# Kernel optimization log

Measured on AMD Instinct MI355X. Metric: run time of the kernel, lower is better.

Reference implementation:

```python
import jax, jax.numpy as jnp
import numpy as np

B = 16384
IN = 512
A = 16
E = 9  # 9 position-specific experts
H1, H2, H3 = 512, 256, 128


def setup_inputs() -> dict:
    key = jax.random.key(0)
    ks = jax.random.split(key, 10)
    s = lambda fan_in: 1.0 / np.sqrt(fan_in)
    return {
        "x": jax.random.normal(ks[0], (B, IN), dtype=jnp.float32),
        "position": jax.random.randint(ks[1], (B,), 0, 9, dtype=jnp.int64),
        # torch Linear convention: W [out, in], y = x @ W.T + b; stacked per expert [E, out, in]
        "W1": jax.random.uniform(ks[2], (E, H1, IN), jnp.float32, -s(IN), s(IN)),
        "b1": jax.random.uniform(ks[3], (E, H1), jnp.float32, -s(IN), s(IN)),
        "W2": jax.random.uniform(ks[4], (E, H2, H1), jnp.float32, -s(H1), s(H1)),
        "b2": jax.random.uniform(ks[5], (E, H2), jnp.float32, -s(H1), s(H1)),
        "W3": jax.random.uniform(ks[6], (E, H3, H2), jnp.float32, -s(H2), s(H2)),
        "b3": jax.random.uniform(ks[7], (E, H3), jnp.float32, -s(H2), s(H2)),
        "W4": jax.random.uniform(ks[8], (E, A, H3), jnp.float32, -s(H3), s(H3)),
        "b4": jax.random.uniform(ks[9], (E, A), jnp.float32, -s(H3), s(H3)),
    }


def reference(x, position, W1, b1, W2, b2, W3, b3, W4, b4):
    # Each sample i is routed through expert min(position[i], 8).
    # Dense MoE reference: run all 9 experts over the full batch, then
    # select the routed expert's logits per sample (same math as the
    # per-sample Python loop in the original module).
    pos = jnp.minimum(position, 8)
    h = jax.nn.relu(jnp.einsum('bi,eoi->ebo', x, W1) + b1[:, None, :])   # [E,B,H1]
    h = jax.nn.relu(jnp.einsum('ebi,eoi->ebo', h, W2) + b2[:, None, :])  # [E,B,H2]
    h = jax.nn.relu(jnp.einsum('ebi,eoi->ebo', h, W3) + b3[:, None, :])  # [E,B,H3]
    logits_all = jnp.einsum('ebi,eoi->ebo', h, W4) + b4[:, None, :]      # [E,B,A]
    logits = logits_all[pos, jnp.arange(x.shape[0])]                     # [B,A]
    return jax.nn.softmax(logits, axis=1)
```

## Files before the change

kernel.cpp:

```cpp
#include <hip/hip_runtime.h>

typedef _Float16 f16;
typedef __attribute__((ext_vector_type(8))) _Float16 f16x8;
typedef __attribute__((ext_vector_type(4))) _Float16 f16x4;
typedef __attribute__((ext_vector_type(4))) float f32x4;

#define MFMA16(a, b, c) __builtin_amdgcn_mfma_f32_16x16x32_f16(a, b, c, 0, 0, 0)

#define B_N 16384
#define E_N 9
#define TILE 32
#define NTILE_MAX 520
#define THREADS 512

#define D_IN 512
#define D_H1 512
#define D_H2 256
#define D_H3 128
#define D_A 16

#define RPW 104
#define O4B 7667712
#define WPL_BYTES 7704576
#define WSLOTS (WPL_BYTES / 16)

#define IDX_OFF 64
#define WP_OFF 131584

#define H2_OFF 32768
#define RING_OFF 49152
#define LDS_BYTES 73728


__global__ void k_bucket(const int* __restrict__ pos, int* __restrict__ hdr,
                         int* __restrict__ idx) {
  __shared__ int cnt[E_N], cur[E_N];
  __shared__ int flag_s;
  const int t = threadIdx.x;
  if (t < E_N) cnt[t] = 0;
  if (t == 0) {
    int nz = 0;
    for (int i = 0; i < 64; ++i) nz |= pos[2 * i + 1];
    flag_s = (nz == 0) ? 1 : 0;
  }
  __syncthreads();
  const bool f64 = flag_s != 0;
  int e[16];
#pragma unroll
  for (int k = 0; k < 16; ++k) {
    int i = k * 1024 + t;
    long long v = f64 ? ((const long long*)pos)[i] : (long long)pos[i];
    v = v < 0 ? 0 : (v > 8 ? 8 : v);
    e[k] = (int)v;
    atomicAdd(&cnt[e[k]], 1);
  }
  __syncthreads();
  if (t == 0) {
    int acc = 0;
    for (int ee = 0; ee < E_N; ++ee) { cur[ee] = acc; acc += cnt[ee]; }
  }
  if (t < E_N) hdr[8 + t] = cnt[t];
  __syncthreads();
#pragma unroll
  for (int k = 0; k < 16; ++k) {
    int i = k * 1024 + t;
    int slot = atomicAdd(&cur[e[k]], 1);
    idx[slot] = i;
  }
}


__global__ void k_wcvt(const float* __restrict__ W1, const float* __restrict__ W2,
                       const float* __restrict__ W3, const float* __restrict__ W4,
                       char* __restrict__ wp) {
  int slot = blockIdx.x * 256 + threadIdx.x;
  if (slot >= WSLOTS) return;
  long addr = (long)slot << 4;
  int lane = slot & 63;
  int lg = lane >> 4, ln = lane & 15;
  const float* src;
  if (addr < O4B) {
    int rec = (int)(addr >> 10);
    int f = rec % RPW;
    int ew = rec / RPW;
    int w = ew & 7, e = ew >> 3;
    if (f < 64) {
      int kk = f >> 2, nf = f & 3;
      int n = w * 64 + nf * 16 + ln;
      int k = kk * 32 + lg * 8;
      src = W1 + ((long)e * D_H1 + n) * D_IN + k;
    } else if (f < 96) {
      int j = f - 64;
      int kk = j >> 1, nf = j & 1;
      int n = w * 32 + nf * 16 + ln;
      int k = kk * 32 + lg * 8;
      src = W2 + ((long)e * D_H2 + n) * D_H1 + k;
    } else {
      int kk = f - 96;
      int n = w * 16 + ln;
      int k = kk * 32 + lg * 8;
      src = W3 + ((long)e * D_H3 + n) * D_H2 + k;
    }
  } else {
    long rel = addr - O4B;
    int e = (int)(rel >> 12);
    int r2 = (int)(rel & 4095);
    int s = r2 >> 4, n = s >> 4, k16 = s & 15;
    src = W4 + ((long)e * D_A + n) * D_H3 + k16 * 8;
  }
  float4 a = *(const float4*)src;
  float4 b = *(const float4*)(src + 4);
  f16x8 h;
  h[0] = (f16)a.x; h[1] = (f16)a.y; h[2] = (f16)a.z; h[3] = (f16)a.w;
  h[4] = (f16)b.x; h[5] = (f16)b.y; h[6] = (f16)b.z; h[7] = (f16)b.w;
  *(f16x8*)(wp + addr) = h;
}


__device__ __forceinline__ f16x8 afrag(const char* base, int strideB, int rowoff,
                                       int kbytes, int lane) {
  int m = rowoff + (lane & 15);
  int q = kbytes + ((lane >> 4) * 16);
  return *(const f16x8*)(base + m * strideB + (q ^ ((m & 15) << 4)));
}

__device__ __forceinline__ void dma16(const char* g, char* l) {
  __builtin_amdgcn_global_load_lds(
      (const __attribute__((address_space(1))) void*)g,
      (__attribute__((address_space(3))) void*)l, 16, 0, 0);
}

template <int N> __device__ __forceinline__ void waitv();
template <> __device__ __forceinline__ void waitv<2>() {
  asm volatile("s_waitcnt vmcnt(2)" ::: "memory");
}
template <> __device__ __forceinline__ void waitv<1>() {
  asm volatile("s_waitcnt vmcnt(1)" ::: "memory");
}
template <> __device__ __forceinline__ void waitv<0>() {
  asm volatile("s_waitcnt vmcnt(0)" ::: "memory");
}

__launch_bounds__(THREADS, 2)
__global__ void k_mlp(const float* __restrict__ x,
                      const float* __restrict__ b1, const float* __restrict__ b2,
                      const float* __restrict__ b3, const float* __restrict__ b4,
                      const int* __restrict__ hdr, const int* __restrict__ idx,
                      const char* __restrict__ wp, float* __restrict__ out) {
  __shared__ __align__(16) char lds[LDS_BYTES];

  int b = blockIdx.x;
  int bswz = (b & 7) * (NTILE_MAX / 8) + (b >> 3);

  const int* counts = hdr + 8;
  int e = -1, tile = 0, base = 0, ne = 0;
  {
    int acc = 0, off = 0;
    for (int ee = 0; ee < E_N; ++ee) {
      int n = counts[ee];
      int nt = (n + TILE - 1) / TILE;
      if (bswz < acc + nt) { e = ee; tile = bswz - acc; ne = n; base = off; break; }
      acc += nt; off += n;
    }
  }
  if (e < 0) return;
  const int rvalid = min(TILE, ne - tile * TILE);
  const int row0 = base + tile * TILE;

  const int t = threadIdx.x;
  const int lane = t & 63;
  const int wid = t >> 6;
  const int lg = lane >> 4;
  const int ln = lane & 15;

  const char* wb = wp + ((long)(e * 8 + wid) * RPW << 10);
  const char* wpe4 = wp + O4B + (long)e * 4096;
  char* ringw = lds + RING_OFF + wid * 3072;

  dma16(wb + 0 * 1024 + lane * 16, ringw + 0 * 1024);
  dma16(wb + 1 * 1024 + lane * 16, ringw + 1 * 1024);
  dma16(wb + 2 * 1024 + lane * 16, ringw + 2 * 1024);

  const float4* x4 = (const float4*)x;
#pragma unroll
  for (int v8 = 0; v8 < 8; ++v8) {
    int u = v8 * THREADS + t;
    int s = u >> 7, c4 = u & 127;
    float4 v = make_float4(0.f, 0.f, 0.f, 0.f);
    if (s < rvalid) v = x4[(long)idx[row0 + s] * (D_IN / 4) + c4];
    f16x4 h;
    h[0] = (f16)v.x; h[1] = (f16)v.y; h[2] = (f16)v.z; h[3] = (f16)v.w;
    *(f16x4*)(lds + s * 1024 + ((c4 * 8) ^ ((s & 15) << 4))) = h;
  }
  __syncthreads();

  {
    f32x4 acc[2][4];
#pragma unroll
    for (int m = 0; m < 2; ++m)
#pragma unroll
      for (int nf = 0; nf < 4; ++nf) acc[m][nf] = (f32x4){0.f, 0.f, 0.f, 0.f};

#pragma unroll
    for (int kk = 0; kk < 16; ++kk) {
      f16x8 A0 = afrag(lds, 1024, 0, kk * 64, lane);
      f16x8 A1 = afrag(lds, 1024, 16, kk * 64, lane);
#pragma unroll
      for (int nf = 0; nf < 4; ++nf) {
        const int rec = kk * 4 + nf;
        waitv<2>();
        f16x8 B = *(const f16x8*)(ringw + (rec % 3) * 1024 + lane * 16);
        __builtin_amdgcn_s_setprio(1);
        acc[0][nf] = MFMA16(A0, B, acc[0][nf]);
        acc[1][nf] = MFMA16(A1, B, acc[1][nf]);
        __builtin_amdgcn_s_setprio(0);
        const int nr = rec + 3;
        dma16(wb + (long)nr * 1024 + lane * 16, ringw + (nr % 3) * 1024);
      }
    }
    __syncthreads();

#pragma unroll
    for (int nf = 0; nf < 4; ++nf) {
      int n = wid * 64 + nf * 16 + ln;
      float bias = b1[e * D_H1 + n];
#pragma unroll
      for (int m = 0; m < 2; ++m)
#pragma unroll
        for (int j = 0; j < 4; ++j) {
          float v = acc[m][nf][j] + bias;
          v = v > 0.f ? v : 0.f;
          int rw = m * 16 + lg * 4 + j;
          *(f16*)(lds + rw * 1024 + ((n * 2) ^ ((rw & 15) << 4))) = (f16)v;
        }
    }
  }
  __syncthreads();

  {
    f32x4 acc2[2][2];
#pragma unroll
    for (int m = 0; m < 2; ++m)
#pragma unroll
      for (int nf = 0; nf < 2; ++nf) acc2[m][nf] = (f32x4){0.f, 0.f, 0.f, 0.f};

#pragma unroll
    for (int kk = 0; kk < 16; ++kk) {
      f16x8 A0 = afrag(lds, 1024, 0, kk * 64, lane);
      f16x8 A1 = afrag(lds, 1024, 16, kk * 64, lane);
#pragma unroll
      for (int nf = 0; nf < 2; ++nf) {
        const int rec = 64 + kk * 2 + nf;
        waitv<2>();
        f16x8 B = *(const f16x8*)(ringw + (rec % 3) * 1024 + lane * 16);
        __builtin_amdgcn_s_setprio(1);
        acc2[0][nf] = MFMA16(A0, B, acc2[0][nf]);
        acc2[1][nf] = MFMA16(A1, B, acc2[1][nf]);
        __builtin_amdgcn_s_setprio(0);
        const int nr = rec + 3;
        dma16(wb + (long)nr * 1024 + lane * 16, ringw + (nr % 3) * 1024);
      }
    }
#pragma unroll
    for (int nf = 0; nf < 2; ++nf) {
      int n = wid * 32 + nf * 16 + ln;
      float bias = b2[e * D_H2 + n];
#pragma unroll
      for (int m = 0; m < 2; ++m)
#pragma unroll
        for (int j = 0; j < 4; ++j) {
          float v = acc2[m][nf][j] + bias;
          v = v > 0.f ? v : 0.f;
          int rw = m * 16 + lg * 4 + j;
          *(f16*)(lds + H2_OFF + rw * 512 + ((n * 2) ^ ((rw & 15) << 4))) = (f16)v;
        }
    }
  }
  __syncthreads();

  {
    f32x4 acc3[2];
    acc3[0] = (f32x4){0.f, 0.f, 0.f, 0.f};
    acc3[1] = (f32x4){0.f, 0.f, 0.f, 0.f};

#define L3STEP(REC, WAITN)                                                     \
  {                                                                            \
    const int kk3 = (REC) - 96;                                                \
    f16x8 A0 = afrag(lds + H2_OFF, 512, 0, kk3 * 64, lane);                    \
    f16x8 A1 = afrag(lds + H2_OFF, 512, 16, kk3 * 64, lane);                   \
    waitv<WAITN>();                                                            \
    f16x8 B = *(const f16x8*)(ringw + ((REC) % 3) * 1024 + lane * 16);         \
    __builtin_amdgcn_s_setprio(1);                                             \
    acc3[0] = MFMA16(A0, B, acc3[0]);                                          \
    acc3[1] = MFMA16(A1, B, acc3[1]);                                          \
    __builtin_amdgcn_s_setprio(0);                                             \
    if ((REC) + 3 <= 103)                                                      \
      dma16(wb + (long)((REC) + 3) * 1024 + lane * 16,                         \
            ringw + (((REC) + 3) % 3) * 1024);                                 \
  }

    L3STEP(96, 2)
    L3STEP(97, 2)
    L3STEP(98, 2)
    L3STEP(99, 2)
    L3STEP(100, 2)
    L3STEP(101, 2)
    L3STEP(102, 1)
    L3STEP(103, 0)
#undef L3STEP

    int n = wid * 16 + ln;
    float bias = b3[e * D_H3 + n];
#pragma unroll
    for (int m = 0; m < 2; ++m)
#pragma unroll
      for (int j = 0; j < 4; ++j) {
        float v = acc3[m][j] + bias;
        v = v > 0.f ? v : 0.f;
        int rw = m * 16 + lg * 4 + j;
        *(f16*)(lds + rw * 256 + ((n * 2) ^ ((rw & 15) << 4))) = (f16)v;
      }
  }
  __syncthreads();

  if (wid < 2) {
    f32x4 a4 = (f32x4){0.f, 0.f, 0.f, 0.f};
#pragma unroll
    for (int kc = 0; kc < 4; ++kc) {
      f16x8 Bv = *(const f16x8*)(wpe4 + ln * 256 + kc * 64 + lg * 16);
      f16x8 Av = afrag(lds, 256, wid * 16, kc * 64, lane);
      a4 = MFMA16(Av, Bv, a4);
    }
    float bias = b4[e * D_A + ln];
#pragma unroll
    for (int j = 0; j < 4; ++j) {
      float v = a4[j] + bias;
      float mx = v;
      for (int msk = 8; msk >= 1; msk >>= 1) mx = fmaxf(mx, __shfl_xor(mx, msk));
      float pe = expf(v - mx);
      float sm = pe;
      for (int msk = 8; msk >= 1; msk >>= 1) sm += __shfl_xor(sm, msk);
      int rl = wid * 16 + lg * 4 + j;
      if (rl < rvalid) out[(long)idx[row0 + rl] * D_A + ln] = pe / sm;
    }
  }
}


extern "C" void kernel_launch(void* const* d_in, const int* in_sizes, int n_in,
                              void* d_out, int out_size, void* d_ws, size_t ws_size,
                              hipStream_t stream) {
  const float* x  = (const float*)d_in[0];
  const int* pos  = (const int*)d_in[1];
  const float* W1 = (const float*)d_in[2];
  const float* b1 = (const float*)d_in[3];
  const float* W2 = (const float*)d_in[4];
  const float* b2 = (const float*)d_in[5];
  const float* W3 = (const float*)d_in[6];
  const float* b3 = (const float*)d_in[7];
  const float* W4 = (const float*)d_in[8];
  const float* b4 = (const float*)d_in[9];
  float* out = (float*)d_out;

  int* hdr = (int*)d_ws;
  int* idx = hdr + IDX_OFF;
  char* wp = (char*)d_ws + WP_OFF;

  hipLaunchKernelGGL(k_bucket, dim3(1), dim3(1024), 0, stream, pos, hdr, idx);
  hipLaunchKernelGGL(k_wcvt, dim3(WSLOTS / 256), dim3(256), 0, stream,
                     W1, W2, W3, W4, wp);
  hipLaunchKernelGGL(k_mlp, dim3(NTILE_MAX), dim3(THREADS), 0, stream,
                     x, b1, b2, b3, b4, hdr, idx, wp, out);
}
```

Measured before the change: 67.94 us.

## Use 16 waves per block with register-prefetched weight fragments instead of LDS DMA ring

Doubles the block to 1024 threads so each of 16 waves owns half as many output columns per layer, and repacks the weight layout into per-wave record streams (56 records for the first 8 waves, 48 for the rest, which skip layer 3). The LDS ring fed by global_load_lds DMA with explicit vmcnt waits is replaced by a 4-deep register queue of direct global loads, which frees 24KB of LDS. The aim is more latency hiding and less LDS traffic and waiting per wave. The cost is higher register pressure at 1024 threads with launch bounds of 2 blocks, idle waves during layer 3, and reliance on the compiler to schedule the waits for the register loads.

```diff
diff --git a/kernel.cpp b/kernel.cpp
--- a/kernel.cpp
+++ b/kernel.cpp
@@ -11,7 +11,7 @@
 #define E_N 9
 #define TILE 32
 #define NTILE_MAX 520
-#define THREADS 512
+#define THREADS 1024
 
 #define D_IN 512
 #define D_H1 512
@@ -19,7 +19,6 @@
 #define D_H3 128
 #define D_A 16
 
-#define RPW 104
 #define O4B 7667712
 #define WPL_BYTES 7704576
 #define WSLOTS (WPL_BYTES / 16)
@@ -28,8 +27,7 @@
 #define WP_OFF 131584
 
 #define H2_OFF 32768
-#define RING_OFF 49152
-#define LDS_BYTES 73728
+#define LDS_BYTES 49152
 
 
 __global__ void k_bucket(const int* __restrict__ pos, int* __restrict__ hdr,
@@ -76,29 +74,27 @@
   int slot = blockIdx.x * 256 + threadIdx.x;
   if (slot >= WSLOTS) return;
   long addr = (long)slot << 4;
-  int lane = slot & 63;
+  int lane = (int)((addr >> 4) & 63);
   int lg = lane >> 4, ln = lane & 15;
   const float* src;
   if (addr < O4B) {
     int rec = (int)(addr >> 10);
-    int f = rec % RPW;
-    int ew = rec / RPW;
-    int w = ew & 7, e = ew >> 3;
-    if (f < 64) {
-      int kk = f >> 2, nf = f & 3;
-      int n = w * 64 + nf * 16 + ln;
-      int k = kk * 32 + lg * 8;
+    int e = rec / 832;
+    int q = rec - e * 832;
+    int s, r;
+    if (q < 448) { s = q / 56; r = q - s * 56; }
+    else { int q2 = q - 448; s = 8 + q2 / 48; r = q2 - (s - 8) * 48; }
+    if (r < 32) {
+      int n = s * 32 + (r & 1) * 16 + ln;
+      int k = (r >> 1) * 32 + lg * 8;
       src = W1 + ((long)e * D_H1 + n) * D_IN + k;
-    } else if (f < 96) {
-      int j = f - 64;
-      int kk = j >> 1, nf = j & 1;
-      int n = w * 32 + nf * 16 + ln;
-      int k = kk * 32 + lg * 8;
+    } else if (r < 48) {
+      int n = s * 16 + ln;
+      int k = (r - 32) * 32 + lg * 8;
       src = W2 + ((long)e * D_H2 + n) * D_H1 + k;
     } else {
-      int kk = f - 96;
-      int n = w * 16 + ln;
-      int k = kk * 32 + lg * 8;
+      int n = (s & 7) * 16 + ln;
+      int k = (r - 48) * 32 + lg * 8;
       src = W3 + ((long)e * D_H3 + n) * D_H2 + k;
     }
   } else {
@@ -124,21 +120,8 @@
   return *(const f16x8*)(base + m * strideB + (q ^ ((m & 15) << 4)));
 }
 
-__device__ __forceinline__ void dma16(const char* g, char* l) {
-  __builtin_amdgcn_global_load_lds(
-      (const __attribute__((address_space(1))) void*)g,
-      (__attribute__((address_space(3))) void*)l, 16, 0, 0);
-}
-
-template <int N> __device__ __forceinline__ void waitv();
-template <> __device__ __forceinline__ void waitv<2>() {
-  asm volatile("s_waitcnt vmcnt(2)" ::: "memory");
-}
-template <> __device__ __forceinline__ void waitv<1>() {
-  asm volatile("s_waitcnt vmcnt(1)" ::: "memory");
-}
-template <> __device__ __forceinline__ void waitv<0>() {
-  asm volatile("s_waitcnt vmcnt(0)" ::: "memory");
+__device__ __forceinline__ f16x8 ldfrag(const char* wb, int f, int lane) {
+  return *(const f16x8*)(wb + (long)f * 1024 + lane * 16);
 }
 
 __launch_bounds__(THREADS, 2)
@@ -173,17 +156,19 @@
   const int lg = lane >> 4;
   const int ln = lane & 15;
 
-  const char* wb = wp + ((long)(e * 8 + wid) * RPW << 10);
+  const char* wb = wp + ((long)e * 832 +
+                         (wid < 8 ? wid * 56 : 448 + (wid - 8) * 48)) * 1024;
   const char* wpe4 = wp + O4B + (long)e * 4096;
-  char* ringw = lds + RING_OFF + wid * 3072;
-
-  dma16(wb + 0 * 1024 + lane * 16, ringw + 0 * 1024);
-  dma16(wb + 1 * 1024 + lane * 16, ringw + 1 * 1024);
-  dma16(wb + 2 * 1024 + lane * 16, ringw + 2 * 1024);
+
+  f16x8 Q[4];
+  Q[0] = ldfrag(wb, 0, lane);
+  Q[1] = ldfrag(wb, 1, lane);
+  Q[2] = ldfrag(wb, 2, lane);
+  Q[3] = ldfrag(wb, 3, lane);
 
   const float4* x4 = (const float4*)x;
 #pragma unroll
-  for (int v8 = 0; v8 < 8; ++v8) {
+  for (int v8 = 0; v8 < 4; ++v8) {
     int u = v8 * THREADS + t;
     int s = u >> 7, c4 = u & 127;
     float4 v = make_float4(0.f, 0.f, 0.f, 0.f);
@@ -194,121 +179,91 @@
   }
   __syncthreads();
 
+  f32x4 acc[2][2];
+#pragma unroll
+  for (int m = 0; m < 2; ++m)
+#pragma unroll
+    for (int nf = 0; nf < 2; ++nf) acc[m][nf] = (f32x4){0.f, 0.f, 0.f, 0.f};
+
+#pragma unroll
+  for (int kk = 0; kk < 16; ++kk) {
+    f16x8 A0 = afrag(lds, 1024, 0, kk * 64, lane);
+    f16x8 A1 = afrag(lds, 1024, 16, kk * 64, lane);
+#pragma unroll
+    for (int nf = 0; nf < 2; ++nf) {
+      const int r = kk * 2 + nf;
+      f16x8 B = Q[r & 3];
+      __builtin_amdgcn_s_setprio(1);
+      acc[0][nf] = MFMA16(A0, B, acc[0][nf]);
+      acc[1][nf] = MFMA16(A1, B, acc[1][nf]);
+      __builtin_amdgcn_s_setprio(0);
+      Q[r & 3] = ldfrag(wb, r + 4, lane);
+    }
+  }
+  __syncthreads();
+
+#pragma unroll
+  for (int nf = 0; nf < 2; ++nf) {
+    int n = wid * 32 + nf * 16 + ln;
+    float bias = b1[e * D_H1 + n];
+#pragma unroll
+    for (int m = 0; m < 2; ++m)
+#pragma unroll
+      for (int j = 0; j < 4; ++j) {
+        float v = acc[m][nf][j] + bias;
+        v = v > 0.f ? v : 0.f;
+        int rw = m * 16 + lg * 4 + j;
+        *(f16*)(lds + rw * 1024 + ((n * 2) ^ ((rw & 15) << 4))) = (f16)v;
+      }
+  }
+  __syncthreads();
+
   {
-    f32x4 acc[2][4];
-#pragma unroll
-    for (int m = 0; m < 2; ++m)
-#pragma unroll
-      for (int nf = 0; nf < 4; ++nf) acc[m][nf] = (f32x4){0.f, 0.f, 0.f, 0.f};
-
+    f32x4 acc2[2];
+    acc2[0] = (f32x4){0.f, 0.f, 0.f, 0.f};
+    acc2[1] = (f32x4){0.f, 0.f, 0.f, 0.f};
 #pragma unroll
     for (int kk = 0; kk < 16; ++kk) {
       f16x8 A0 = afrag(lds, 1024, 0, kk * 64, lane);
       f16x8 A1 = afrag(lds, 1024, 16, kk * 64, lane);
-#pragma unroll
-      for (int nf = 0; nf < 4; ++nf) {
-        const int rec = kk * 4 + nf;
-        waitv<2>();
-        f16x8 B = *(const f16x8*)(ringw + (rec % 3) * 1024 + lane * 16);
-        __builtin_amdgcn_s_setprio(1);
-        acc[0][nf] = MFMA16(A0, B, acc[0][nf]);
-        acc[1][nf] = MFMA16(A1, B, acc[1][nf]);
-        __builtin_amdgcn_s_setprio(0);
-        const int nr = rec + 3;
-        dma16(wb + (long)nr * 1024 + lane * 16, ringw + (nr % 3) * 1024);
+      const int r = 32 + kk;
+      f16x8 B = Q[r & 3];
+      __builtin_amdgcn_s_setprio(1);
+      acc2[0] = MFMA16(A0, B, acc2[0]);
+      acc2[1] = MFMA16(A1, B, acc2[1]);
+      __builtin_amdgcn_s_setprio(0);
+      Q[r & 3] = ldfrag(wb, r + 4, lane);
+    }
+    int n = wid * 16 + ln;
+    float bias = b2[e * D_H2 + n];
+#pragma unroll
+    for (int m = 0; m < 2; ++m)
+#pragma unroll
+      for (int j = 0; j < 4; ++j) {
+        float v = acc2[m][j] + bias;
+        v = v > 0.f ? v : 0.f;
+        int rw = m * 16 + lg * 4 + j;
+        *(f16*)(lds + H2_OFF + rw * 512 + ((n * 2) ^ ((rw & 15) << 4))) = (f16)v;
       }
-    }
-    __syncthreads();
-
-#pragma unroll
-    for (int nf = 0; nf < 4; ++nf) {
-      int n = wid * 64 + nf * 16 + ln;
-      float bias = b1[e * D_H1 + n];
-#pragma unroll
-      for (int m = 0; m < 2; ++m)
-#pragma unroll
-        for (int j = 0; j < 4; ++j) {
-          float v = acc[m][nf][j] + bias;
-          v = v > 0.f ? v : 0.f;
-          int rw = m * 16 + lg * 4 + j;
-          *(f16*)(lds + rw * 1024 + ((n * 2) ^ ((rw & 15) << 4))) = (f16)v;
-        }
-    }
-  }
-  __syncthreads();
-
-  {
-    f32x4 acc2[2][2];
-#pragma unroll
-    for (int m = 0; m < 2; ++m)
-#pragma unroll
-      for (int nf = 0; nf < 2; ++nf) acc2[m][nf] = (f32x4){0.f, 0.f, 0.f, 0.f};
-
-#pragma unroll
-    for (int kk = 0; kk < 16; ++kk) {
-      f16x8 A0 = afrag(lds, 1024, 0, kk * 64, lane);
-      f16x8 A1 = afrag(lds, 1024, 16, kk * 64, lane);
-#pragma unroll
-      for (int nf = 0; nf < 2; ++nf) {
-        const int rec = 64 + kk * 2 + nf;
-        waitv<2>();
-        f16x8 B = *(const f16x8*)(ringw + (rec % 3) * 1024 + lane * 16);
-        __builtin_amdgcn_s_setprio(1);
-        acc2[0][nf] = MFMA16(A0, B, acc2[0][nf]);
-        acc2[1][nf] = MFMA16(A1, B, acc2[1][nf]);
-        __builtin_amdgcn_s_setprio(0);
-        const int nr = rec + 3;
-        dma16(wb + (long)nr * 1024 + lane * 16, ringw + (nr % 3) * 1024);
-      }
-    }
-#pragma unroll
-    for (int nf = 0; nf < 2; ++nf) {
-      int n = wid * 32 + nf * 16 + ln;
-      float bias = b2[e * D_H2 + n];
-#pragma unroll
-      for (int m = 0; m < 2; ++m)
-#pragma unroll
-        for (int j = 0; j < 4; ++j) {
-          float v = acc2[m][nf][j] + bias;
-          v = v > 0.f ? v : 0.f;
-          int rw = m * 16 + lg * 4 + j;
-          *(f16*)(lds + H2_OFF + rw * 512 + ((n * 2) ^ ((rw & 15) << 4))) = (f16)v;
-        }
-    }
-  }
-  __syncthreads();
-
-  {
+  }
+  __syncthreads();
+
+  if (wid < 8) {
     f32x4 acc3[2];
     acc3[0] = (f32x4){0.f, 0.f, 0.f, 0.f};
     acc3[1] = (f32x4){0.f, 0.f, 0.f, 0.f};
-
-#define L3STEP(REC, WAITN)                                                     \
-  {                                                                            \
-    const int kk3 = (REC) - 96;                                                \
-    f16x8 A0 = afrag(lds + H2_OFF, 512, 0, kk3 * 64, lane);                    \
-    f16x8 A1 = afrag(lds + H2_OFF, 512, 16, kk3 * 64, lane);                   \
-    waitv<WAITN>();                                                            \
-    f16x8 B = *(const f16x8*)(ringw + ((REC) % 3) * 1024 + lane * 16);         \
-    __builtin_amdgcn_s_setprio(1);                                             \
-    acc3[0] = MFMA16(A0, B, acc3[0]);                                          \
-    acc3[1] = MFMA16(A1, B, acc3[1]);                                          \
-    __builtin_amdgcn_s_setprio(0);                                             \
-    if ((REC) + 3 <= 103)                                                      \
-      dma16(wb + (long)((REC) + 3) * 1024 + lane * 16,                         \
-            ringw + (((REC) + 3) % 3) * 1024);                                 \
-  }
-
-    L3STEP(96, 2)
-    L3STEP(97, 2)
-    L3STEP(98, 2)
-    L3STEP(99, 2)
-    L3STEP(100, 2)
-    L3STEP(101, 2)
-    L3STEP(102, 1)
-    L3STEP(103, 0)
-#undef L3STEP
-
+#pragma unroll
+    for (int kk = 0; kk < 8; ++kk) {
+      const int r = 48 + kk;
+      f16x8 A0 = afrag(lds + H2_OFF, 512, 0, kk * 64, lane);
+      f16x8 A1 = afrag(lds + H2_OFF, 512, 16, kk * 64, lane);
+      f16x8 B = Q[r & 3];
+      __builtin_amdgcn_s_setprio(1);
+      acc3[0] = MFMA16(A0, B, acc3[0]);
+      acc3[1] = MFMA16(A1, B, acc3[1]);
+      __builtin_amdgcn_s_setprio(0);
+      if (r + 4 <= 55) Q[r & 3] = ldfrag(wb, r + 4, lane);
+    }
     int n = wid * 16 + ln;
     float bias = b3[e * D_H3 + n];
 #pragma unroll
```

After: 70.86 us. 4.3% more time.

## Split fused per-tile MLP into per-layer grouped GEMMs with 128-row tiles

Applied to the files above, without the earlier changes.

Replaces the single fused 32-row-tile MLP kernel with a pipeline: an x gather/convert kernel into a padded, swizzled fp16 buffer, three grouped GEMM kernels (128x128 tiles, double-buffered LDS) that convert weights inline, and a scalar layer-4 softmax kernel. Larger row tiles raise weight reuse per load and remove the separate weight pre-conversion pass. In exchange it adds intermediate activation round-trips through global memory and extra launches. The fused path is kept as a fallback when the workspace is too small.

```diff
diff --git a/kernel.cpp b/kernel.cpp
--- a/kernel.cpp
+++ b/kernel.cpp
@@ -9,9 +9,8 @@
 
 #define B_N 16384
 #define E_N 9
-#define TILE 32
-#define NTILE_MAX 520
-#define THREADS 512
+#define MAXT 144
+#define MP_MAX 17536
 
 #define D_IN 512
 #define D_H1 512
@@ -19,17 +18,41 @@
 #define D_H3 128
 #define D_A 16
 
-#define RPW 104
-#define O4B 7667712
-#define WPL_BYTES 7704576
-#define WSLOTS (WPL_BYTES / 16)
-
-#define IDX_OFF 64
-#define WP_OFF 131584
-
-#define H2_OFF 32768
-#define RING_OFF 49152
-#define LDS_BYTES 73728
+#define IDX_I 64
+#define SIDX_B 65792
+#define XG_B 136192
+#define H1_B 18093056
+#define H2_B 136192
+#define H3_B 9114624
+#define WS_NEED_PIPE 36049920ull
+#define F_RPW 104
+#define F_O4B 7667712
+#define F_WPL 7704576
+#define F_WSLOTS (F_WPL / 16)
+#define F_WP_OFF 131584
+#define F_H2_OFF 32768
+#define F_RING_OFF 49152
+#define F_LDS 73728
+#define F_NTILE 520
+
+
+
+__device__ __forceinline__ void dma16(const char* g, char* l) {
+  __builtin_amdgcn_global_load_lds(
+      (const __attribute__((address_space(1))) void*)g,
+      (__attribute__((address_space(3))) void*)l, 16, 0, 0);
+}
+
+template <int N> __device__ __forceinline__ void waitv();
+template <> __device__ __forceinline__ void waitv<2>() {
+  asm volatile("s_waitcnt vmcnt(2)" ::: "memory");
+}
+template <> __device__ __forceinline__ void waitv<1>() {
+  asm volatile("s_waitcnt vmcnt(1)" ::: "memory");
+}
+template <> __device__ __forceinline__ void waitv<0>() {
+  asm volatile("s_waitcnt vmcnt(0)" ::: "memory");
+}
 
 
 __global__ void k_bucket(const int* __restrict__ pos, int* __restrict__ hdr,
@@ -56,10 +79,22 @@
   }
   __syncthreads();
   if (t == 0) {
-    int acc = 0;
-    for (int ee = 0; ee < E_N; ++ee) { cur[ee] = acc; acc += cnt[ee]; }
-  }
-  if (t < E_N) hdr[8 + t] = cnt[t];
+    int ua = 0, pa = 0, ta = 0;
+    for (int ee = 0; ee < E_N; ++ee) {
+      cur[ee] = ua;
+      hdr[8 + ee] = cnt[ee];
+      hdr[20 + ee] = ua;
+      hdr[32 + ee] = pa;
+      hdr[44 + ee] = ta;
+      int c = cnt[ee];
+      ua += c;
+      int tl = (c + 127) >> 7;
+      pa += tl << 7;
+      ta += tl;
+    }
+    hdr[32 + 9] = pa;
+    hdr[44 + 9] = ta;
+  }
   __syncthreads();
 #pragma unroll
   for (int k = 0; k < 16; ++k) {
@@ -70,19 +105,221 @@
 }
 
 
-__global__ void k_wcvt(const float* __restrict__ W1, const float* __restrict__ W2,
-                       const float* __restrict__ W3, const float* __restrict__ W4,
-                       char* __restrict__ wp) {
+__global__ void k_xcvt(const float* __restrict__ x, const int* __restrict__ hdr,
+                       const int* __restrict__ idx, char* __restrict__ xg,
+                       int* __restrict__ sidx) {
+  const int* cnt = hdr + 8;
+  const int* uoff = hdr + 20;
+  const int* pof = hdr + 32;
+  const int Mp = pof[9];
+  int gtid = blockIdx.x * 256 + threadIdx.x;
+
+  if (gtid < MP_MAX) {
+    int v = -1;
+    if (gtid < Mp) {
+      int e = 0;
+#pragma unroll
+      for (int ee = 1; ee < E_N; ++ee) if (gtid >= pof[ee]) e = ee;
+      int i = gtid - pof[e];
+      if (i < cnt[e]) v = idx[uoff[e] + i];
+    }
+    sidx[gtid] = v;
+  }
+
+  if (gtid >= Mp * 64) return;
+  long L = (long)gtid << 4;
+  int c = (int)(L >> 14);
+  int tile = c >> 3, ks = c & 7;
+  int r = (int)((L >> 7) & 127);
+  int pos = (int)(L & 127);
+  int slot = (tile << 7) + r;
+  int klog = pos ^ ((r & 7) << 4);
+  int k = (ks << 6) + (klog >> 1);
+
+  int e = 0;
+#pragma unroll
+  for (int ee = 1; ee < E_N; ++ee) if (slot >= pof[ee]) e = ee;
+  int i = slot - pof[e];
+  f16x8 h;
+  if (i < cnt[e]) {
+    int orig = idx[uoff[e] + i];
+    const float* src = x + (long)orig * D_IN + k;
+    float4 a = *(const float4*)src;
+    float4 b = *(const float4*)(src + 4);
+    h[0] = (f16)a.x; h[1] = (f16)a.y; h[2] = (f16)a.z; h[3] = (f16)a.w;
+    h[4] = (f16)b.x; h[5] = (f16)b.y; h[6] = (f16)b.z; h[7] = (f16)b.w;
+  } else {
+#pragma unroll
+    for (int q = 0; q < 8; ++q) h[q] = (f16)0.f;
+  }
+  *(f16x8*)(xg + L) = h;
+}
+
+__device__ __forceinline__ f16x8 afragP(const char* base, int rowoff, int kbytes,
+                                        int lane) {
+  int m = rowoff + (lane & 15);
+  int q = kbytes + ((lane >> 4) * 16);
+  return *(const f16x8*)(base + m * 128 + (q ^ ((m & 7) << 4)));
+}
+
+template <int K, int NTN>
+__launch_bounds__(512, 2)
+__global__ void k_gemm(const char* __restrict__ Ag, const float* __restrict__ W,
+                       const float* __restrict__ bias, const int* __restrict__ hdr,
+                       char* __restrict__ Og) {
+  constexpr int NOUT = NTN * 128;
+  constexpr int S = K / 64;
+  constexpr int OCH = NOUT / 64;
+  __shared__ __align__(16) char lds[65536];
+
+  const int* pof = hdr + 32;
+  const int* ptil = hdr + 44;
+  int nb = blockIdx.x;
+  int tb = nb / NTN, nt = nb % NTN;
+  if (tb >= ptil[9]) return;
+  int e = 0;
+#pragma unroll
+  for (int ee = 1; ee < E_N; ++ee) if (tb >= ptil[ee]) e = ee;
+  const int slot0 = pof[e] + (tb - ptil[e]) * 128;
+
+  const int t = threadIdx.x;
+  const int lane = t & 63;
+  const int wid = t >> 6;
+  const int lg = lane >> 4;
+  const int ln = lane & 15;
+  const int mw = wid >> 1;
+  const int nw = wid & 1;
+
+  const char* Abase = Ag + (((long)(slot0 >> 7) * S) << 14);
+
+  auto stageA = [&](int s, int p) {
+    const char* src = Abase + ((long)s << 14) + wid * 1024 + lane * 16;
+    char* d0 = lds + p * 16384 + wid * 1024;
+    dma16(src, d0);
+    dma16(src + 8192, d0 + 8192);
+  };
+  auto stageW = [&](int s, int p) {
+    char* wd = lds + 32768 + p * 16384;
+#pragma unroll
+    for (int j = 0; j < 2; ++j) {
+      int q = t + j * 512;
+      int col = q >> 3, kb16 = q & 7;
+      int klog = (kb16 * 16) ^ ((col & 7) << 4);
+      int k = s * 64 + (klog >> 1);
+      const float* wsrc = W + ((long)(e * NOUT + nt * 128 + col) * K + k);
+      float4 a = *(const float4*)wsrc;
+      float4 b = *(const float4*)(wsrc + 4);
+      f16x8 h;
+      h[0] = (f16)a.x; h[1] = (f16)a.y; h[2] = (f16)a.z; h[3] = (f16)a.w;
+      h[4] = (f16)b.x; h[5] = (f16)b.y; h[6] = (f16)b.z; h[7] = (f16)b.w;
+      *(f16x8*)(wd + q * 16) = h;
+    }
+  };
+
+  f32x4 acc[2][4];
+#pragma unroll
+  for (int m2 = 0; m2 < 2; ++m2)
+#pragma unroll
+    for (int nf = 0; nf < 4; ++nf) acc[m2][nf] = (f32x4){0.f, 0.f, 0.f, 0.f};
+
+  stageA(0, 0);
+  stageW(0, 0);
+  __syncthreads();
+
+  for (int s = 0; s < S; ++s) {
+    const int p = s & 1;
+    if (s + 1 < S) { stageA(s + 1, p ^ 1); stageW(s + 1, p ^ 1); }
+    const char* Ap = lds + p * 16384;
+    const char* Wp = lds + 32768 + p * 16384;
+#pragma unroll
+    for (int ks = 0; ks < 2; ++ks) {
+      f16x8 A0 = afragP(Ap, mw * 32, ks * 64, lane);
+      f16x8 A1 = afragP(Ap, mw * 32 + 16, ks * 64, lane);
+#pragma unroll
+      for (int nf = 0; nf < 4; ++nf) {
+        f16x8 B = afragP(Wp, nw * 64 + nf * 16, ks * 64, lane);
+        acc[0][nf] = MFMA16(A0, B, acc[0][nf]);
+        acc[1][nf] = MFMA16(A1, B, acc[1][nf]);
+      }
+    }
+    __syncthreads();
+  }
+
+#pragma unroll
+  for (int nf = 0; nf < 4; ++nf) {
+    int cg = nt * 128 + nw * 64 + nf * 16 + ln;
+    float bb = bias[e * NOUT + cg];
+#pragma unroll
+    for (int m2 = 0; m2 < 2; ++m2)
+#pragma unroll
+      for (int j = 0; j < 4; ++j) {
+        float v = acc[m2][nf][j] + bb;
+        v = v > 0.f ? v : 0.f;
+        int row = mw * 32 + m2 * 16 + lg * 4 + j;
+        int slot = slot0 + row;
+        long byte = ((long)((slot >> 7) * OCH + (cg >> 6)) << 14) +
+                    (long)(slot & 127) * 128 +
+                    (((cg & 63) * 2) ^ ((slot & 7) << 4));
+        *(f16*)(Og + byte) = (f16)v;
+      }
+  }
+}
+
+__global__ void k_l4(const char* __restrict__ h3, const float* __restrict__ W4,
+                     const float* __restrict__ b4, const int* __restrict__ hdr,
+                     const int* __restrict__ sidx, float* __restrict__ out) {
+  const int* pof = hdr + 32;
+  const int* ptil = hdr + 44;
+  int tb = blockIdx.x;
+  if (tb >= ptil[9]) return;
+  int e = 0;
+#pragma unroll
+  for (int ee = 1; ee < E_N; ++ee) if (tb >= ptil[ee]) e = ee;
+  const int slot0 = pof[e] + (tb - ptil[e]) * 128;
+
+  const int t = threadIdx.x;
+  const int rr = t >> 4, a = t & 15;
+#pragma unroll
+  for (int g = 0; g < 8; ++g) {
+    int slot = slot0 + g * 16 + rr;
+    float accv = b4[e * D_A + a];
+#pragma unroll
+    for (int c = 0; c < 16; ++c) {
+      long byte = ((long)((slot >> 7) * 2 + (c >> 3)) << 14) +
+                  (long)(slot & 127) * 128 +
+                  (((c & 7) * 16) ^ ((slot & 7) << 4));
+      f16x8 h = *(const f16x8*)(h3 + byte);
+      const float* w = W4 + ((long)(e * D_A + a) * D_H3 + c * 8);
+      float4 wa = *(const float4*)w;
+      float4 wb = *(const float4*)(w + 4);
+      accv += (float)h[0] * wa.x + (float)h[1] * wa.y + (float)h[2] * wa.z +
+              (float)h[3] * wa.w + (float)h[4] * wb.x + (float)h[5] * wb.y +
+              (float)h[6] * wb.z + (float)h[7] * wb.w;
+    }
+    float mx = accv;
+    for (int msk = 8; msk >= 1; msk >>= 1) mx = fmaxf(mx, __shfl_xor(mx, msk, 16));
+    float pe = expf(accv - mx);
+    float sm = pe;
+    for (int msk = 8; msk >= 1; msk >>= 1) sm += __shfl_xor(sm, msk, 16);
+    int orig = sidx[slot];
+    if (orig >= 0) out[(long)orig * D_A + a] = pe / sm;
+  }
+}
+
+
+__global__ void k_wcvt_f(const float* __restrict__ W1, const float* __restrict__ W2,
+                         const float* __restrict__ W3, const float* __restrict__ W4,
+                         char* __restrict__ wp) {
   int slot = blockIdx.x * 256 + threadIdx.x;
-  if (slot >= WSLOTS) return;
+  if (slot >= F_WSLOTS) return;
   long addr = (long)slot << 4;
   int lane = slot & 63;
   int lg = lane >> 4, ln = lane & 15;
   const float* src;
-  if (addr < O4B) {
+  if (addr < F_O4B) {
     int rec = (int)(addr >> 10);
-    int f = rec % RPW;
-    int ew = rec / RPW;
+    int f = rec % F_RPW;
+    int ew = rec / F_RPW;
     int w = ew & 7, e = ew >> 3;
     if (f < 64) {
       int kk = f >> 2, nf = f & 3;
@@ -102,7 +339,7 @@
       src = W3 + ((long)e * D_H3 + n) * D_H2 + k;
     }
   } else {
-    long rel = addr - O4B;
+    long rel = addr - F_O4B;
     int e = (int)(rel >> 12);
     int r2 = (int)(rel & 4095);
     int s = r2 >> 4, n = s >> 4, k16 = s & 15;
@@ -116,41 +353,23 @@
   *(f16x8*)(wp + addr) = h;
 }
 
-
-__device__ __forceinline__ f16x8 afrag(const char* base, int strideB, int rowoff,
-                                       int kbytes, int lane) {
+__device__ __forceinline__ f16x8 afragS(const char* base, int strideB, int rowoff,
+                                        int kbytes, int lane) {
   int m = rowoff + (lane & 15);
   int q = kbytes + ((lane >> 4) * 16);
   return *(const f16x8*)(base + m * strideB + (q ^ ((m & 15) << 4)));
 }
 
-__device__ __forceinline__ void dma16(const char* g, char* l) {
-  __builtin_amdgcn_global_load_lds(
-      (const __attribute__((address_space(1))) void*)g,
-      (__attribute__((address_space(3))) void*)l, 16, 0, 0);
-}
-
-template <int N> __device__ __forceinline__ void waitv();
-template <> __device__ __forceinline__ void waitv<2>() {
-  asm volatile("s_waitcnt vmcnt(2)" ::: "memory");
-}
-template <> __device__ __forceinline__ void waitv<1>() {
-  asm volatile("s_waitcnt vmcnt(1)" ::: "memory");
-}
-template <> __device__ __forceinline__ void waitv<0>() {
-  asm volatile("s_waitcnt vmcnt(0)" ::: "memory");
-}
-
-__launch_bounds__(THREADS, 2)
-__global__ void k_mlp(const float* __restrict__ x,
-                      const float* __restrict__ b1, const float* __restrict__ b2,
-                      const float* __restrict__ b3, const float* __restrict__ b4,
-                      const int* __restrict__ hdr, const int* __restrict__ idx,
-                      const char* __restrict__ wp, float* __restrict__ out) {
-  __shared__ __align__(16) char lds[LDS_BYTES];
+__launch_bounds__(512, 2)
+__global__ void k_mlp_f(const float* __restrict__ x,
+                        const float* __restrict__ b1, const float* __restrict__ b2,
+                        const float* __restrict__ b3, const float* __restrict__ b4,
+                        const int* __restrict__ hdr, const int* __restrict__ idx,
+                        const char* __restrict__ wp, float* __restrict__ out) {
+  __shared__ __align__(16) char lds[F_LDS];
 
   int b = blockIdx.x;
-  int bswz = (b & 7) * (NTILE_MAX / 8) + (b >> 3);
+  int bswz = (b & 7) * (F_NTILE / 8) + (b >> 3);
 
   const int* counts = hdr + 8;
   int e = -1, tile = 0, base = 0, ne = 0;
@@ -158,14 +377,14 @@
     int acc = 0, off = 0;
     for (int ee = 0; ee < E_N; ++ee) {
       int n = counts[ee];
-      int nt = (n + TILE - 1) / TILE;
+      int nt = (n + 31) / 32;
       if (bswz < acc + nt) { e = ee; tile = bswz - acc; ne = n; base = off; break; }
       acc += nt; off += n;
     }
   }
   if (e < 0) return;
-  const int rvalid = min(TILE, ne - tile * TILE);
-  const int row0 = base + tile * TILE;
+  const int rvalid = min(32, ne - tile * 32);
+  const int row0 = base + tile * 32;
 
   const int t = threadIdx.x;
   const int lane = t & 63;
@@ -173,9 +392,9 @@
   const int lg = lane >> 4;
   const int ln = lane & 15;
 
-  const char* wb = wp + ((long)(e * 8 + wid) * RPW << 10);
-  const char* wpe4 = wp + O4B + (long)e * 4096;
-  char* ringw = lds + RING_OFF + wid * 3072;
+  const char* wb = wp + ((long)(e * 8 + wid) * F_RPW << 10);
+  const char* wpe4 = wp + F_O4B + (long)e * 4096;
+  char* ringw = lds + F_RING_OFF + wid * 3072;
 
   dma16(wb + 0 * 1024 + lane * 16, ringw + 0 * 1024);
   dma16(wb + 1 * 1024 + lane * 16, ringw + 1 * 1024);
@@ -184,7 +403,7 @@
   const float4* x4 = (const float4*)x;
 #pragma unroll
   for (int v8 = 0; v8 < 8; ++v8) {
-    int u = v8 * THREADS + t;
+    int u = v8 * 512 + t;
     int s = u >> 7, c4 = u & 127;
     float4 v = make_float4(0.f, 0.f, 0.f, 0.f);
     if (s < rvalid) v = x4[(long)idx[row0 + s] * (D_IN / 4) + c4];
@@ -203,8 +422,8 @@
 
 #pragma unroll
     for (int kk = 0; kk < 16; ++kk) {
-      f16x8 A0 = afrag(lds, 1024, 0, kk * 64, lane);
-      f16x8 A1 = afrag(lds, 1024, 16, kk * 64, lane);
+      f16x8 A0 = afragS(lds, 1024, 0, kk * 64, lane);
+      f16x8 A1 = afragS(lds, 1024, 16, kk * 64, lane);
 #pragma unroll
       for (int nf = 0; nf < 4; ++nf) {
         const int rec = kk * 4 + nf;
@@ -246,8 +465,8 @@
 
 #pragma unroll
     for (int kk = 0; kk < 16; ++kk) {
-      f16x8 A0 = afrag(lds, 1024, 0, kk * 64, lane);
-      f16x8 A1 = afrag(lds, 1024, 16, kk * 64, lane);
+      f16x8 A0 = afragS(lds, 1024, 0, kk * 64, lane);
+      f16x8 A1 = afragS(lds, 1024, 16, kk * 64, lane);
 #pragma unroll
       for (int nf = 0; nf < 2; ++nf) {
         const int rec = 64 + kk * 2 + nf;
@@ -272,7 +491,7 @@
           float v = acc2[m][nf][j] + bias;
           v = v > 0.f ? v : 0.f;
           int rw = m * 16 + lg * 4 + j;
-          *(f16*)(lds + H2_OFF + rw * 512 + ((n * 2) ^ ((rw & 15) << 4))) = (f16)v;
+          *(f16*)(lds + F_H2_OFF + rw * 512 + ((n * 2) ^ ((rw & 15) << 4))) = (f16)v;
         }
     }
   }
@@ -286,8 +505,8 @@
 #define L3STEP(REC, WAITN)                                                     \
   {                                                                            \
     const int kk3 = (REC) - 96;                                                \
-    f16x8 A0 = afrag(lds + H2_OFF, 512, 0, kk3 * 64, lane);                    \
-    f16x8 A1 = afrag(lds + H2_OFF, 512, 16, kk3 * 64, lane);                   \
+    f16x8 A0 = afragS(lds + F_H2_OFF, 512, 0, kk3 * 64, lane);                 \
+    f16x8 A1 = afragS(lds + F_H2_OFF, 512, 16, kk3 * 64, lane);                \
     waitv<WAITN>();                                                            \
     f16x8 B = *(const f16x8*)(ringw + ((REC) % 3) * 1024 + lane * 16);         \
     __builtin_amdgcn_s_setprio(1);                                             \
@@ -328,7 +547,7 @@
 #pragma unroll
     for (int kc = 0; kc < 4; ++kc) {
       f16x8 Bv = *(const f16x8*)(wpe4 + ln * 256 + kc * 64 + lg * 16);
-      f16x8 Av = afrag(lds, 256, wid * 16, kc * 64, lane);
+      f16x8 Av = afragS(lds, 256, wid * 16, kc * 64, lane);
       a4 = MFMA16(Av, Bv, a4);
     }
     float bias = b4[e * D_A + ln];
@@ -363,12 +582,31 @@
   float* out = (float*)d_out;
 
   int* hdr = (int*)d_ws;
-  int* idx = hdr + IDX_OFF;
-  char* wp = (char*)d_ws + WP_OFF;
+  int* idx = hdr + IDX_I;
 
   hipLaunchKernelGGL(k_bucket, dim3(1), dim3(1024), 0, stream, pos, hdr, idx);
-  hipLaunchKernelGGL(k_wcvt, dim3(WSLOTS / 256), dim3(256), 0, stream,
-                     W1, W2, W3, W4, wp);
-  hipLaunchKernelGGL(k_mlp, dim3(NTILE_MAX), dim3(THREADS), 0, stream,
-                     x, b1, b2, b3, b4, hdr, idx, wp, out);
-}
+
+  if (ws_size >= WS_NEED_PIPE) {
+    int* sidx = (int*)((char*)d_ws + SIDX_B);
+    char* xg = (char*)d_ws + XG_B;
+    char* h1 = (char*)d_ws + H1_B;
+    char* h2 = (char*)d_ws + H2_B;
+    char* h3 = (char*)d_ws + H3_B;
+    hipLaunchKernelGGL(k_xcvt, dim3((MP_MAX * 64) / 256), dim3(256), 0, stream,
+                       x, hdr, idx, xg, sidx);
+    hipLaunchKernelGGL((k_gemm<512, 4>), dim3(MAXT * 4), dim3(512), 0, stream,
+                       xg, W1, b1, hdr, h1);
+    hipLaunchKernelGGL((k_gemm<512, 2>), dim3(MAXT * 2), dim3(512), 0, stream,
+                       h1, W2, b2, hdr, h2);
+    hipLaunchKernelGGL((k_gemm<256, 1>), dim3(MAXT), dim3(512), 0, stream,
+                       h2, W3, b3, hdr, h3);
+    hipLaunchKernelGGL(k_l4, dim3(MAXT), dim3(256), 0, stream,
+                       h3, W4, b4, hdr, sidx, out);
+  } else {
+    char* wp = (char*)d_ws + F_WP_OFF;
+    hipLaunchKernelGGL(k_wcvt_f, dim3(F_WSLOTS / 256), dim3(256), 0, stream,
+                       W1, W2, W3, W4, wp);
+    hipLaunchKernelGGL(k_mlp_f, dim3(F_NTILE), dim3(512), 0, stream,
+                       x, b1, b2, b3, b4, hdr, idx, wp, out);
+  }
+}
```

After: 127.1 us. 87.1% more time.
